# Performance work log

Measured on AMD Instinct MI355X. Metric: run time of the kernel, lower is better.

The kernel has to match this reference:

```python
import jax, jax.numpy as jnp
import numpy as np

ALPHA = 0.65  # self.alpha
B, L = 4096, 4096


def setup_inputs() -> dict:
    key = jax.random.key(0)
    k1, k2 = jax.random.split(key)
    output = jax.random.normal(k1, (B, L, 2), dtype=jnp.float32)
    labels = jax.random.randint(k2, (B, L), 0, 2, dtype=jnp.int32)
    return {"output": output, "labels": labels}


def reference(output, labels):
    # output: [B, L, 2] (channel 0 = truncate, channel 1 = continue); labels: [B, L] in {0,1}
    Bn, Ln, _ = output.shape
    # --- slice_index, vectorized over the batch ---
    temp = jnp.argmax(output, axis=-1)                    # [B, L] in {0,1}
    all_ones = jnp.all(temp == 1, axis=1)                 # [B]
    # index of the last 0 in temp[i]: L-1 - (first-min index of the flipped row)
    k = jnp.argmin(temp[:, ::-1], axis=1)                 # [B]
    cut = jnp.where(all_ones, Ln, Ln - 1 - k)             # [B]; mask[i, cut:] = 0
    mask = (jnp.arange(Ln)[None, :] < cut[:, None]).astype(output.dtype)  # [B, L]
    # --- reward tensor r (metric='nci'): r[...,0] = 0 always, r[...,1] depends on label ---
    j = jnp.arange(Ln, dtype=output.dtype)
    pos_reward = -3.6 / jnp.log2(j + 2.0)                 # [L]
    r1 = jnp.where(labels == 1, pos_reward[None, :], ALPHA * 0.1)  # [B, L]
    # sum(output * mask * r) / B; only channel 1 contributes since r[...,0] == 0
    loss = jnp.sum(output[..., 1] * mask * r1) / Bn
    return loss
```

## Files before the change

kernel.cpp:

```cpp
#include <hip/hip_runtime.h>


#define LROW 4096
#define BROW 4096
#define BDIM 256
#define KITER (LROW / 2 / BDIM)

__global__ __launch_bounds__(BDIM, 2) void bicut_partial_kernel(
    const float* __restrict__ out,
    const int* __restrict__ labels,
    float* __restrict__ partial) {
    const int row = blockIdx.x;
    const int tid = threadIdx.x;
    const float4* rowp4 = reinterpret_cast<const float4*>(out + (size_t)row * 2 * LROW);
    const int2* labp2 = reinterpret_cast<const int2*>(labels + (size_t)row * LROW);

    float4 o[KITER];
    int2 lb[KITER];
#pragma unroll
    for (int k = 0; k < KITER; ++k) o[k] = rowp4[k * BDIM + tid];
#pragma unroll
    for (int k = 0; k < KITER; ++k) lb[k] = labp2[k * BDIM + tid];

    int zmax = -1;
#pragma unroll
    for (int k = 0; k < KITER; ++k) {
        const int p = k * BDIM + tid;
        if (!(o[k].y > o[k].x)) zmax = 2 * p;
        if (!(o[k].w > o[k].z)) zmax = 2 * p + 1;
    }

    __shared__ int smax[BDIM / 64];
    __shared__ float ssum[BDIM / 64];
    const int wid = tid >> 6, lane = tid & 63;
#pragma unroll
    for (int off = 32; off; off >>= 1) zmax = max(zmax, __shfl_down(zmax, off));
    if (lane == 0) smax[wid] = zmax;
    __syncthreads();
    const int mall = max(max(smax[0], smax[1]), max(smax[2], smax[3]));
    const int cut = (mall < 0) ? LROW : mall;

    float s = 0.0f;
#pragma unroll
    for (int k = 0; k < KITER; ++k) {
        const int p = k * BDIM + tid;
        const int j0 = 2 * p, j1 = j0 + 1;
        const float pr0 = -3.6f * __builtin_amdgcn_rcpf(__log2f((float)j0 + 2.0f));
        const float pr1 = -3.6f * __builtin_amdgcn_rcpf(__log2f((float)j1 + 2.0f));
        const float t0 = o[k].y * ((lb[k].x == 1) ? pr0 : 0.065f);
        const float t1 = o[k].w * ((lb[k].y == 1) ? pr1 : 0.065f);
        if (j0 < cut) s += t0;
        if (j1 < cut) s += t1;
    }
#pragma unroll
    for (int off = 32; off; off >>= 1) s += __shfl_down(s, off);
    if (lane == 0) ssum[wid] = s;
    __syncthreads();
    if (tid == 0)
        partial[row] = ssum[0] + ssum[1] + ssum[2] + ssum[3];
}

__global__ __launch_bounds__(256) void bicut_final_kernel(
    const float* __restrict__ partial,
    float* __restrict__ loss) {
    const int tid = threadIdx.x;
    const float4* p4 = reinterpret_cast<const float4*>(partial);
    float s = 0.0f;
#pragma unroll
    for (int k = 0; k < BROW / 4 / 256; ++k) {
        const float4 v = p4[k * 256 + tid];
        s += v.x + v.y + v.z + v.w;
    }
    __shared__ float ss[4];
    const int wid = tid >> 6, lane = tid & 63;
#pragma unroll
    for (int off = 32; off; off >>= 1) s += __shfl_down(s, off);
    if (lane == 0) ss[wid] = s;
    __syncthreads();
    if (tid == 0) loss[0] = (ss[0] + ss[1] + ss[2] + ss[3]) * (1.0f / (float)BROW);
}

extern "C" void kernel_launch(void* const* d_in, const int* in_sizes, int n_in,
                              void* d_out, int out_size, void* d_ws, size_t ws_size,
                              hipStream_t stream) {
    const float* out = (const float*)d_in[0];
    const int* labels = (const int*)d_in[1];
    float* loss = (float*)d_out;
    float* partial = (float*)d_ws;

    bicut_partial_kernel<<<BROW, BDIM, 0, stream>>>(out, labels, partial);
    bicut_final_kernel<<<1, 256, 0, stream>>>(partial, loss);
}
```

Baseline: 230.8 us.

## Split row reduction into per-segment partials plus boundary fixup pass

Replaces the one-block-per-row kernel with a flat kernel where each wavefront covers a 256-element segment and records both the last-zero index and the unmasked partial sum. A second kernel combines the 16 segment records per row, keeps only the segments lying fully before the cut, and recomputes the single straddling segment from global memory. This removes the per-row block barrier and register-heavy staging, giving many small independent blocks. The cost is an extra launch, workspace traffic, and a partial re-read of one segment per row.

Result: no change. 234.2 us (+1.5%).

```diff
diff --git a/kernel.cpp b/kernel.cpp
--- a/kernel.cpp
+++ b/kernel.cpp
@@ -3,61 +3,85 @@
 
 #define LROW 4096
 #define BROW 4096
-#define BDIM 256
-#define KITER (LROW / 2 / BDIM)
+#define ALPHA_R 0.065f
 
-__global__ __launch_bounds__(BDIM, 2) void bicut_partial_kernel(
+__device__ __forceinline__ float reward(int lab, int jl) {
+    const float pr = -3.6f * __builtin_amdgcn_rcpf(__log2f((float)jl + 2.0f));
+    return (lab == 1) ? pr : ALPHA_R;
+}
+
+__global__ __launch_bounds__(256) void bicut_k1(
     const float* __restrict__ out,
     const int* __restrict__ labels,
-    float* __restrict__ partial) {
-    const int row = blockIdx.x;
-    const int tid = threadIdx.x;
-    const float4* rowp4 = reinterpret_cast<const float4*>(out + (size_t)row * 2 * LROW);
-    const int2* labp2 = reinterpret_cast<const int2*>(labels + (size_t)row * LROW);
+    int2* __restrict__ recs) {
+    const int b = blockIdx.x;
+    const int t = threadIdx.x;
+    const int e0 = (b << 10) + (t << 2);
+    const float4* o4 = reinterpret_cast<const float4*>(out);
+    const int4* l4 = reinterpret_cast<const int4*>(labels);
 
-    float4 o[KITER];
-    int2 lb[KITER];
+    const float4 a = o4[e0 >> 1];
+    const float4 c = o4[(e0 >> 1) + 1];
+    const int4 lb = l4[e0 >> 2];
+
+    const int jl = e0 & (LROW - 1);
+    int zm = -1;
+    if (!(a.y > a.x)) zm = jl;
+    if (!(a.w > a.z)) zm = jl + 1;
+    if (!(c.y > c.x)) zm = jl + 2;
+    if (!(c.w > c.z)) zm = jl + 3;
+
+    float s = a.y * reward(lb.x, jl)
+            + a.w * reward(lb.y, jl + 1)
+            + c.y * reward(lb.z, jl + 2)
+            + c.w * reward(lb.w, jl + 3);
+
 #pragma unroll
-    for (int k = 0; k < KITER; ++k) o[k] = rowp4[k * BDIM + tid];
+    for (int off = 32; off; off >>= 1) {
+        zm = max(zm, __shfl_down(zm, off));
+        s += __shfl_down(s, off);
+    }
+    if ((t & 63) == 0)
+        recs[(b << 2) + (t >> 6)] = make_int2(zm, __float_as_int(s));
+}
+
+__global__ __launch_bounds__(256) void bicut_k2(
+    const float* __restrict__ out,
+    const int* __restrict__ labels,
+    const int2* __restrict__ recs,
+    float* __restrict__ rowsum) {
+    const int lane = threadIdx.x & 63;
+    const int wid = threadIdx.x >> 6;
+    const int r = (blockIdx.x << 2) + wid;
+
+    const int w = lane & 15;
+    const int2 rec = recs[r * 16 + w];
+    int zm = rec.x;
 #pragma unroll
-    for (int k = 0; k < KITER; ++k) lb[k] = labp2[k * BDIM + tid];
+    for (int off = 32; off; off >>= 1) zm = max(zm, __shfl_down(zm, off));
+    zm = __shfl(zm, 0);
+    const int cut = (zm < 0) ? LROW : zm;
 
-    int zmax = -1;
-#pragma unroll
-    for (int k = 0; k < KITER; ++k) {
-        const int p = k * BDIM + tid;
-        if (!(o[k].y > o[k].x)) zmax = 2 * p;
-        if (!(o[k].w > o[k].z)) zmax = 2 * p + 1;
+    float s = (lane < 16 && (w + 1) * 256 <= cut) ? __int_as_float(rec.y) : 0.0f;
+
+    if (cut & 255) {
+        const int mb = cut >> 8;
+        const int j0 = (mb << 8) + (lane << 2);
+        const int e0 = r * LROW + j0;
+        const float4* o4 = reinterpret_cast<const float4*>(out);
+        const int4* l4 = reinterpret_cast<const int4*>(labels);
+        const float4 a = o4[e0 >> 1];
+        const float4 c = o4[(e0 >> 1) + 1];
+        const int4 lb = l4[e0 >> 2];
+        if (j0 + 0 < cut) s += a.y * reward(lb.x, j0);
+        if (j0 + 1 < cut) s += a.w * reward(lb.y, j0 + 1);
+        if (j0 + 2 < cut) s += c.y * reward(lb.z, j0 + 2);
+        if (j0 + 3 < cut) s += c.w * reward(lb.w, j0 + 3);
     }
 
-    __shared__ int smax[BDIM / 64];
-    __shared__ float ssum[BDIM / 64];
-    const int wid = tid >> 6, lane = tid & 63;
-#pragma unroll
-    for (int off = 32; off; off >>= 1) zmax = max(zmax, __shfl_down(zmax, off));
-    if (lane == 0) smax[wid] = zmax;
-    __syncthreads();
-    const int mall = max(max(smax[0], smax[1]), max(smax[2], smax[3]));
-    const int cut = (mall < 0) ? LROW : mall;
-
-    float s = 0.0f;
-#pragma unroll
-    for (int k = 0; k < KITER; ++k) {
-        const int p = k * BDIM + tid;
-        const int j0 = 2 * p, j1 = j0 + 1;
-        const float pr0 = -3.6f * __builtin_amdgcn_rcpf(__log2f((float)j0 + 2.0f));
-        const float pr1 = -3.6f * __builtin_amdgcn_rcpf(__log2f((float)j1 + 2.0f));
-        const float t0 = o[k].y * ((lb[k].x == 1) ? pr0 : 0.065f);
-        const float t1 = o[k].w * ((lb[k].y == 1) ? pr1 : 0.065f);
-        if (j0 < cut) s += t0;
-        if (j1 < cut) s += t1;
-    }
 #pragma unroll
     for (int off = 32; off; off >>= 1) s += __shfl_down(s, off);
-    if (lane == 0) ssum[wid] = s;
-    __syncthreads();
-    if (tid == 0)
-        partial[row] = ssum[0] + ssum[1] + ssum[2] + ssum[3];
+    if (lane == 0) rowsum[r] = s;
 }
 
 __global__ __launch_bounds__(256) void bicut_final_kernel(
@@ -86,8 +110,10 @@
     const float* out = (const float*)d_in[0];
     const int* labels = (const int*)d_in[1];
     float* loss = (float*)d_out;
-    float* partial = (float*)d_ws;
+    int2* recs = (int2*)d_ws;
+    float* rowsum = (float*)((char*)d_ws + (1 << 20));
 
-    bicut_partial_kernel<<<BROW, BDIM, 0, stream>>>(out, labels, partial);
-    bicut_final_kernel<<<1, 256, 0, stream>>>(partial, loss);
+    bicut_k1<<<(BROW * LROW) / 1024, 256, 0, stream>>>(out, labels, recs);
+    bicut_k2<<<BROW / 4, 256, 0, stream>>>(out, labels, recs, rowsum);
+    bicut_final_kernel<<<1, 256, 0, stream>>>(rowsum, loss);
 }
```
